# Performance work log

Hardware: AMD Instinct MI355X
Metric: run time of the kernel (lower is better)

Reference implementation:

```python
import jax, jax.numpy as jnp
import numpy as np

WS = 7           # window side
N = WS * WS      # tokens per window = 49
DIM = 384
H = 12
HD = DIM // H    # 32
BW = 2048        # num_windows * batch
NW = 4           # windows per image (mask batch)
SCALE = 1.0 / float(np.sqrt(HD))


def _rel_index():
    coords = np.stack(np.meshgrid(np.arange(WS), np.arange(WS), indexing='ij'))  # (2,7,7)
    flat = coords.reshape(2, -1)                      # (2,49)
    rel = flat[:, :, None] - flat[:, None, :]         # (2,49,49)
    rel = rel.transpose(1, 2, 0).copy()               # (49,49,2)
    rel[..., 0] += WS - 1
    rel[..., 1] += WS - 1
    rel[..., 0] *= 2 * WS - 1
    return jnp.asarray(rel.sum(-1), dtype=jnp.int32)  # (49,49)


def setup_inputs() -> dict:
    key = jax.random.key(0)
    ks = jax.random.split(key, 16)
    f32 = jnp.float32
    se = jax.random.normal(ks[0], (BW, N, DIM), dtype=f32)
    de = jax.random.normal(ks[1], (BW, N, DIM), dtype=f32)
    mask = jnp.where(jax.random.uniform(ks[2], (NW, N, N)) < 0.1, f32(-1e9), f32(0.0))
    s = 0.02
    w_v_se = jax.random.normal(ks[3], (DIM, DIM), dtype=f32) * s
    b_v_se = jnp.zeros((DIM,), dtype=f32)
    w_qkv = jax.random.normal(ks[4], (3 * DIM, DIM), dtype=f32) * s
    b_qkv = jnp.zeros((3 * DIM,), dtype=f32)
    w_proj_se = jax.random.normal(ks[5], (DIM, DIM), dtype=f32) * s
    b_proj_se = jnp.zeros((DIM,), dtype=f32)
    w_proj_de = jax.random.normal(ks[6], (DIM, DIM), dtype=f32) * s
    b_proj_de = jnp.zeros((DIM,), dtype=f32)
    rpb = jax.random.normal(ks[7], ((2 * WS - 1) ** 2, H), dtype=f32) * s  # (169,12)
    rel_idx = _rel_index()
    return {
        'se': se, 'de': de, 'mask': mask,
        'w_v_se': w_v_se, 'b_v_se': b_v_se,
        'w_qkv': w_qkv, 'b_qkv': b_qkv,
        'w_proj_se': w_proj_se, 'b_proj_se': b_proj_se,
        'w_proj_de': w_proj_de, 'b_proj_de': b_proj_de,
        'rpb': rpb, 'rel_idx': rel_idx,
    }


def reference(se, de, mask, w_v_se, b_v_se, w_qkv, b_qkv,
              w_proj_se, b_proj_se, w_proj_de, b_proj_de, rpb, rel_idx):
    B_, N_, C = se.shape
    # qkv from de (coa=False branch)
    qkv = (de @ w_qkv.T + b_qkv).reshape(B_, N_, 3, H, HD).transpose(2, 0, 3, 1, 4)
    q, k, v_de = qkv[0], qkv[1], qkv[2]                 # (B_,H,N,HD)
    v_se = (se @ w_v_se.T + b_v_se).reshape(B_, N_, H, HD).transpose(0, 2, 1, 3)
    attn = jnp.einsum('bhnd,bhmd->bhnm', q * SCALE, k)  # (B_,H,N,N)
    bias = rpb[rel_idx].transpose(2, 0, 1)              # (H,N,N)
    attn = attn + bias[None]
    # add window mask: view as (B, nW, H, N, N)
    attn = attn.reshape(B_ // NW, NW, H, N_, N_) + mask[None, :, None]
    attn = jax.nn.softmax(attn.reshape(B_, H, N_, N_), axis=-1)
    se_o = jnp.einsum('bhnm,bhmd->bnhd', attn, v_se).reshape(B_, N_, C)
    de_o = jnp.einsum('bhnm,bhmd->bnhd', attn, v_de).reshape(B_, N_, C)
    se_o = se_o @ w_proj_se.T + b_proj_se
    de_o = de_o @ w_proj_de.T + b_proj_de
    return (se_o, de_o)
```

## Files before the change

### kernel.cpp

```cpp
#include <hip/hip_runtime.h>

typedef _Float16 f16;
typedef __attribute__((ext_vector_type(8))) _Float16 f16x8;
typedef __attribute__((ext_vector_type(4))) _Float16 f16x4;
typedef __attribute__((ext_vector_type(4))) float f32x4;

#define MFMA16(a, b, c) __builtin_amdgcn_mfma_f32_16x16x32_f16(a, b, c, 0, 0, 0)

#define SCALE_F 0.17677669529663687f
#define NHEAD 12
#define NTOK 49
#define NBW 2048
#define VTJ 56

#define SB() __builtin_amdgcn_s_barrier()
#define SCHEDB() __builtin_amdgcn_sched_barrier(0)
#define WAITL0() asm volatile("s_waitcnt lgkmcnt(0)" ::: "memory")

__global__ void cast_weights(const float* __restrict__ wqkv, const float* __restrict__ wvse,
                             const float* __restrict__ wpse, const float* __restrict__ wpde,
                             f16* o_qkv, f16* o_vse, f16* o_pse, f16* o_pde) {
    int i = blockIdx.x * 256 + threadIdx.x;
    if (i >= 221184) return;
    const float* src;
    f16* dst;
    int off;
    if (i < 110592) { src = wqkv; dst = o_qkv; off = i; }
    else if (i < 147456) { src = wvse; dst = o_vse; off = i - 110592; }
    else if (i < 184320) { src = wpse; dst = o_pse; off = i - 147456; }
    else { src = wpde; dst = o_pde; off = i - 184320; }
    f32x4 v = ((const f32x4*)src)[off];
    f16x4 o;
#pragma unroll
    for (int e = 0; e < 4; ++e) o[e] = (f16)v[e];
    ((f16x4*)dst)[off] = o;
}

__global__ void prep_bm(const float* __restrict__ rpb, const int* __restrict__ rel_idx,
                        const float* __restrict__ mask, float* __restrict__ bm) {
    int blk = blockIdx.x;
    int w4 = blk / NHEAD, h = blk - w4 * NHEAD;
    for (int idx = threadIdx.x; idx < 4096; idx += 64) {
        int r = idx >> 6, c = idx & 63;
        float v = -1e30f;
        if (r < NTOK && c < NTOK)
            v = rpb[rel_idx[r * NTOK + c] * NHEAD + h] + mask[(w4 * NTOK + r) * NTOK + c];
        bm[(size_t)blk * 4096 + idx] = v;
    }
}

template <int EPI, bool A_F32, typename OUT_T>
__global__ __launch_bounds__(256) void gemm_bt(const void* __restrict__ Av, const f16* __restrict__ B,
                                               const float* __restrict__ bias, OUT_T* __restrict__ C,
                                               f16* __restrict__ VT, int N, int ldc) {
    __shared__ __align__(16) f16 As[128 * 64];
    __shared__ __align__(16) f16 Bs[128 * 64];
    const int nwg = gridDim.x * gridDim.y;
    int wg = blockIdx.y * gridDim.x + blockIdx.x;
    wg = (wg & 7) * (nwg >> 3) + (wg >> 3);
    const int m0 = (wg / gridDim.x) * 128, n0 = (wg % gridDim.x) * 128;
    const int tid = threadIdx.x;
    const int w = tid >> 6, l = tid & 63;
    const int wm = w >> 1, wn = w & 1;
    const int lr = l & 15, lg = l >> 4;
    const int sp = l & 7;
    const int lrow = l >> 3;

    f32x4 acc[4][4] = {};
    f32x4 t0[4], t1[4];
    f16x8 tf[4];

    auto LOADA = [&](int kt) {
#pragma unroll
        for (int it = 0; it < 4; ++it) {
            int row = w * 32 + it * 8 + lrow;
            if constexpr (A_F32) {
                const float* g = (const float*)Av + (size_t)(m0 + row) * 384 + kt * 64 + sp * 8;
                t0[it] = *(const f32x4*)g;
                t1[it] = *(const f32x4*)(g + 4);
            } else {
                tf[it] = *(const f16x8*)((const f16*)Av + (size_t)(m0 + row) * 384 + kt * 64 + sp * 8);
            }
        }
    };
    auto CVTWRITE = [&]() {
#pragma unroll
        for (int it = 0; it < 4; ++it) {
            int row = w * 32 + it * 8 + lrow;
            f16x8 hx;
            if constexpr (A_F32) {
#pragma unroll
                for (int e = 0; e < 4; ++e) { hx[e] = (f16)t0[it][e]; hx[e + 4] = (f16)t1[it][e]; }
            } else {
                hx = tf[it];
            }
            *(f16x8*)(As + row * 64 + (sp ^ (row & 7)) * 8) = hx;
        }
    };
    auto STAGEB = [&](int kt) {
#pragma unroll
        for (int it = 0; it < 4; ++it) {
            int row = w * 32 + it * 8 + lrow;
            int gchunk = sp ^ (row & 7);
            const f16* gB = B + (size_t)(n0 + row) * 384 + kt * 64 + gchunk * 8;
            f16* lB = Bs + (w * 32 + it * 8) * 64;
            __builtin_amdgcn_global_load_lds((const __attribute__((address_space(1))) void*)gB,
                                             (__attribute__((address_space(3))) void*)lB, 16, 0, 0);
        }
    };

    LOADA(0);
#pragma unroll
    for (int t = 0; t < 6; ++t) {
        WAITL0();
        SB();
        SCHEDB();
        CVTWRITE();
        STAGEB(t);
        if (t < 5) LOADA(t + 1);
        WAITL0();
        if (t < 5) {
            if constexpr (A_F32) asm volatile("s_waitcnt vmcnt(8)" ::: "memory");
            else asm volatile("s_waitcnt vmcnt(4)" ::: "memory");
        } else {
            asm volatile("s_waitcnt vmcnt(0)" ::: "memory");
        }
        SB();
        SCHEDB();
#pragma unroll
        for (int ks = 0; ks < 2; ++ks) {
            f16x8 af[4], bfr[4];
#pragma unroll
            for (int mi = 0; mi < 4; ++mi) {
                int r = 64 * wm + 16 * mi + lr;
                int chunk = (lg + 4 * ks) ^ (r & 7);
                af[mi] = *(const f16x8*)(As + r * 64 + chunk * 8);
            }
#pragma unroll
            for (int ni = 0; ni < 4; ++ni) {
                int r = 64 * wn + 16 * ni + lr;
                int chunk = (lg + 4 * ks) ^ (r & 7);
                bfr[ni] = *(const f16x8*)(Bs + r * 64 + chunk * 8);
            }
            __builtin_amdgcn_s_setprio(1);
#pragma unroll
            for (int mi = 0; mi < 4; ++mi)
#pragma unroll
                for (int ni = 0; ni < 4; ++ni)
                    acc[mi][ni] = MFMA16(af[mi], bfr[ni], acc[mi][ni]);
            __builtin_amdgcn_s_setprio(0);
        }
    }

#pragma unroll
    for (int mi = 0; mi < 4; ++mi) {
#pragma unroll
        for (int ni = 0; ni < 4; ++ni) {
            int col = n0 + 64 * wn + 16 * ni + lr;
            float bv = bias[col];
#pragma unroll
            for (int reg = 0; reg < 4; ++reg) {
                int row = m0 + 64 * wm + 16 * mi + 4 * lg + reg;
                float v = acc[mi][ni][reg] + bv;
                if constexpr (EPI == 0) {
                    C[(size_t)row * ldc + col] = (OUT_T)v;
                } else if constexpr (EPI == 1) {
                    if (col < 768) {
                        if (col < 384) v *= SCALE_F;
                        C[(size_t)row * 768 + col] = (OUT_T)v;
                    } else {
                        int c2 = col - 768;
                        int b = row / 49, j = row - b * 49;
                        VT[((size_t)b * NHEAD + (c2 >> 5)) * (32 * VTJ) + (c2 & 31) * VTJ + j] = (f16)v;
                    }
                } else {
                    int b = row / 49, j = row - b * 49;
                    VT[((size_t)b * NHEAD + (col >> 5)) * (32 * VTJ) + (col & 31) * VTJ + j] = (f16)v;
                }
            }
        }
    }
}

__global__ __launch_bounds__(128) void attn_kernel(const f16* __restrict__ qk,
                                                   const f16* __restrict__ vse_t,
                                                   const f16* __restrict__ vde_t,
                                                   const float* __restrict__ bm_all,
                                                   f16* __restrict__ att_se, f16* __restrict__ att_de) {
    __shared__ __align__(16) f16 Ps[2][64 * 64];

    const int wv = threadIdx.x >> 6;
    const int l = threadIdx.x & 63;
    const int bh = blockIdx.x * 2 + wv;
    const int b = bh / NHEAD, h = bh - b * NHEAD;
    const int lr = l & 15, lg = l >> 4;
    const size_t wbase = (size_t)b * NTOK;
    f16* P = Ps[wv];

    f16x8 qa[4], kb[4];
#pragma unroll
    for (int mi = 0; mi < 4; ++mi)
        qa[mi] = *(const f16x8*)(qk + (wbase + 16 * mi + lr) * 768 + h * 32 + lg * 8);
#pragma unroll
    for (int ni = 0; ni < 4; ++ni)
        kb[ni] = *(const f16x8*)(qk + (wbase + 16 * ni + lr) * 768 + 384 + h * 32 + lg * 8);

    const f32x4 zero4 = {0.f, 0.f, 0.f, 0.f};
    f32x4 S[4][4];
    __builtin_amdgcn_s_setprio(1);
#pragma unroll
    for (int mi = 0; mi < 4; ++mi)
#pragma unroll
        for (int ni = 0; ni < 4; ++ni)
            S[mi][ni] = MFMA16(qa[mi], kb[ni], zero4);
    __builtin_amdgcn_s_setprio(0);

    f16x8 vbr[2][2][2];
#pragma unroll
    for (int s = 0; s < 2; ++s) {
        const f16* vt = (s ? vde_t : vse_t) + (size_t)bh * (32 * VTJ);
#pragma unroll
        for (int ks = 0; ks < 2; ++ks)
#pragma unroll
            for (int ni = 0; ni < 2; ++ni) {
                int j0 = 8 * lg + 32 * ks;
                if (j0 == 56) j0 = 48;
                vbr[s][ks][ni] = *(const f16x8*)(vt + (16 * ni + lr) * VTJ + j0);
            }
    }

    const float* bmp = bm_all + (size_t)((b & 3) * NHEAD + h) * 4096;
#pragma unroll
    for (int mi = 0; mi < 4; ++mi) {
#pragma unroll
        for (int reg = 0; reg < 4; ++reg) {
            int r = 16 * mi + 4 * lg + reg;
            float v[4];
#pragma unroll
            for (int ni = 0; ni < 4; ++ni)
                v[ni] = S[mi][ni][reg] + bmp[(r << 6) + 16 * ni + lr];
            float mx = fmaxf(fmaxf(v[0], v[1]), fmaxf(v[2], v[3]));
#pragma unroll
            for (int off = 1; off < 16; off <<= 1) mx = fmaxf(mx, __shfl_xor(mx, off));
            float e[4];
            float sm = 0.f;
#pragma unroll
            for (int ni = 0; ni < 4; ++ni) {
                e[ni] = __expf(v[ni] - mx);
                sm += e[ni];
            }
#pragma unroll
            for (int off = 1; off < 16; off <<= 1) sm += __shfl_xor(sm, off);
            float inv = 1.f / sm;
#pragma unroll
            for (int ni = 0; ni < 4; ++ni)
                P[(r << 6) + ((16 * ni + lr) ^ ((r & 7) << 3))] = (f16)(e[ni] * inv);
        }
    }
    WAITL0();
    SCHEDB();

#pragma unroll
    for (int s = 0; s < 2; ++s) {
        f32x4 o[4][2] = {};
#pragma unroll
        for (int ks = 0; ks < 2; ++ks) {
            f16x8 pa[4];
#pragma unroll
            for (int mi = 0; mi < 4; ++mi) {
                int r = 16 * mi + lr;
                pa[mi] = *(const f16x8*)(P + (r << 6) + ((8 * lg + 32 * ks) ^ ((r & 7) << 3)));
            }
            __builtin_amdgcn_s_setprio(1);
#pragma unroll
            for (int ni = 0; ni < 2; ++ni)
#pragma unroll
                for (int mi = 0; mi < 4; ++mi) o[mi][ni] = MFMA16(pa[mi], vbr[s][ks][ni], o[mi][ni]);
            __builtin_amdgcn_s_setprio(0);
        }
        f16* dst = s ? att_de : att_se;
#pragma unroll
        for (int mi = 0; mi < 4; ++mi) {
#pragma unroll
            for (int reg = 0; reg < 4; ++reg) {
                int r = 16 * mi + 4 * lg + reg;
                if (r < NTOK) {
#pragma unroll
                    for (int ni = 0; ni < 2; ++ni)
                        dst[(wbase + r) * 384 + h * 32 + 16 * ni + lr] = (f16)o[mi][ni][reg];
                }
            }
        }
    }
}

extern "C" void kernel_launch(void* const* d_in, const int* in_sizes, int n_in,
                              void* d_out, int out_size, void* d_ws, size_t ws_size,
                              hipStream_t stream) {
    const float* se = (const float*)d_in[0];
    const float* de = (const float*)d_in[1];
    const float* mask = (const float*)d_in[2];
    const float* w_v_se = (const float*)d_in[3];
    const float* b_v_se = (const float*)d_in[4];
    const float* w_qkv = (const float*)d_in[5];
    const float* b_qkv = (const float*)d_in[6];
    const float* w_proj_se = (const float*)d_in[7];
    const float* b_proj_se = (const float*)d_in[8];
    const float* w_proj_de = (const float*)d_in[9];
    const float* b_proj_de = (const float*)d_in[10];
    const float* rpb = (const float*)d_in[11];
    const int* rel_idx = (const int*)d_in[12];

    const size_t SE_ELEMS = (size_t)NBW * NTOK * 384;

    char* ws = (char*)d_ws;
    f16* att_se = (f16*)(ws);
    f16* att_de = (f16*)(ws + 77070336);
    f16* qk_h   = (f16*)(ws + 154140672);
    f16* vse_t  = (f16*)(ws + 308281344);
    f16* vde_t  = (f16*)(ws + 396361728);
    f16* wqkv_h = (f16*)(ws + 484442112);
    f16* wvse_h = (f16*)(ws + 485326848);
    f16* wpse_h = (f16*)(ws + 485621760);
    f16* wpde_h = (f16*)(ws + 485916672);
    float* bm   = (float*)(ws + 486211584);

    cast_weights<<<864, 256, 0, stream>>>(w_qkv, w_v_se, w_proj_se, w_proj_de,
                                          wqkv_h, wvse_h, wpse_h, wpde_h);
    prep_bm<<<48, 64, 0, stream>>>(rpb, rel_idx, mask, bm);

    gemm_bt<1, true, f16><<<dim3(9, 784), 256, 0, stream>>>((const void*)de, wqkv_h, b_qkv,
                                                            qk_h, vde_t, 1152, 768);
    gemm_bt<2, true, f16><<<dim3(3, 784), 256, 0, stream>>>((const void*)se, wvse_h, b_v_se,
                                                            (f16*)nullptr, vse_t, 384, 384);

    attn_kernel<<<NBW * NHEAD / 2, 128, 0, stream>>>(qk_h, vse_t, vde_t, bm, att_se, att_de);

    gemm_bt<0, false, float><<<dim3(3, 784), 256, 0, stream>>>((const void*)att_se, wpse_h, b_proj_se,
                                                               (float*)d_out, nullptr, 384, 384);
    gemm_bt<0, false, float><<<dim3(3, 784), 256, 0, stream>>>((const void*)att_de, wpde_h, b_proj_de,
                                                               (float*)d_out + SE_ELEMS, nullptr, 384, 384);
}
```

Before: 697.6 us.

## Remove register prefetch pipeline in GEMM; use direct global-to-LDS loads for f16 A

The gemm_bt main loop drops its software pipelining, which prefetched the next A tile into registers while computing the current one. Each K-step now loads and converts A synchronously between two __syncthreads. For f16 A inputs, the A tile is also staged straight into LDS with global_load_lds, mirroring B, instead of going through registers. This cuts register pressure and the hand-written waitcnt logic, but global load latency is no longer overlapped with MFMA work.

```diff
diff --git a/kernel.cpp b/kernel.cpp
--- a/kernel.cpp
+++ b/kernel.cpp
@@ -13,7 +13,6 @@
 #define NBW 2048
 #define VTJ 56
 
-#define SB() __builtin_amdgcn_s_barrier()
 #define SCHEDB() __builtin_amdgcn_sched_barrier(0)
 #define WAITL0() asm volatile("s_waitcnt lgkmcnt(0)" ::: "memory")
 
@@ -67,66 +66,53 @@
     const int lrow = l >> 3;
 
     f32x4 acc[4][4] = {};
-    f32x4 t0[4], t1[4];
-    f16x8 tf[4];
-
-    auto LOADA = [&](int kt) {
-#pragma unroll
-        for (int it = 0; it < 4; ++it) {
-            int row = w * 32 + it * 8 + lrow;
-            if constexpr (A_F32) {
-                const float* g = (const float*)Av + (size_t)(m0 + row) * 384 + kt * 64 + sp * 8;
+
+    for (int t = 0; t < 6; ++t) {
+        __syncthreads();
+        if constexpr (A_F32) {
+            const float* A32 = (const float*)Av;
+            f32x4 t0[4], t1[4];
+#pragma unroll
+            for (int it = 0; it < 4; ++it) {
+                int row = w * 32 + it * 8 + lrow;
+                const float* g = A32 + (size_t)(m0 + row) * 384 + t * 64 + sp * 8;
                 t0[it] = *(const f32x4*)g;
                 t1[it] = *(const f32x4*)(g + 4);
-            } else {
-                tf[it] = *(const f16x8*)((const f16*)Av + (size_t)(m0 + row) * 384 + kt * 64 + sp * 8);
-            }
-        }
-    };
-    auto CVTWRITE = [&]() {
-#pragma unroll
-        for (int it = 0; it < 4; ++it) {
-            int row = w * 32 + it * 8 + lrow;
-            f16x8 hx;
-            if constexpr (A_F32) {
+            }
+#pragma unroll
+            for (int it = 0; it < 4; ++it) {
+                int row = w * 32 + it * 8 + lrow;
+                f16x8 hx;
 #pragma unroll
                 for (int e = 0; e < 4; ++e) { hx[e] = (f16)t0[it][e]; hx[e + 4] = (f16)t1[it][e]; }
-            } else {
-                hx = tf[it];
-            }
-            *(f16x8*)(As + row * 64 + (sp ^ (row & 7)) * 8) = hx;
-        }
-    };
-    auto STAGEB = [&](int kt) {
-#pragma unroll
-        for (int it = 0; it < 4; ++it) {
-            int row = w * 32 + it * 8 + lrow;
-            int gchunk = sp ^ (row & 7);
-            const f16* gB = B + (size_t)(n0 + row) * 384 + kt * 64 + gchunk * 8;
-            f16* lB = Bs + (w * 32 + it * 8) * 64;
-            __builtin_amdgcn_global_load_lds((const __attribute__((address_space(1))) void*)gB,
-                                             (__attribute__((address_space(3))) void*)lB, 16, 0, 0);
-        }
-    };
-
-    LOADA(0);
-#pragma unroll
-    for (int t = 0; t < 6; ++t) {
-        WAITL0();
-        SB();
-        SCHEDB();
-        CVTWRITE();
-        STAGEB(t);
-        if (t < 5) LOADA(t + 1);
-        WAITL0();
-        if (t < 5) {
-            if constexpr (A_F32) asm volatile("s_waitcnt vmcnt(8)" ::: "memory");
-            else asm volatile("s_waitcnt vmcnt(4)" ::: "memory");
+                *(f16x8*)(As + row * 64 + (sp ^ (row & 7)) * 8) = hx;
+            }
+#pragma unroll
+            for (int it = 0; it < 4; ++it) {
+                int row = w * 32 + it * 8 + lrow;
+                int gchunk = sp ^ (row & 7);
+                const f16* gB = B + (size_t)(n0 + row) * 384 + t * 64 + gchunk * 8;
+                f16* lB = Bs + (w * 32 + it * 8) * 64;
+                __builtin_amdgcn_global_load_lds((const __attribute__((address_space(1))) void*)gB,
+                                                 (__attribute__((address_space(3))) void*)lB, 16, 0, 0);
+            }
         } else {
-            asm volatile("s_waitcnt vmcnt(0)" ::: "memory");
-        }
-        SB();
-        SCHEDB();
+            const f16* A16 = (const f16*)Av;
+#pragma unroll
+            for (int it = 0; it < 4; ++it) {
+                int row = w * 32 + it * 8 + lrow;
+                int gchunk = sp ^ (row & 7);
+                const f16* gA = A16 + (size_t)(m0 + row) * 384 + t * 64 + gchunk * 8;
+                const f16* gB = B + (size_t)(n0 + row) * 384 + t * 64 + gchunk * 8;
+                f16* lA = As + (w * 32 + it * 8) * 64;
+                f16* lB = Bs + (w * 32 + it * 8) * 64;
+                __builtin_amdgcn_global_load_lds((const __attribute__((address_space(1))) void*)gA,
+                                                 (__attribute__((address_space(3))) void*)lA, 16, 0, 0);
+                __builtin_amdgcn_global_load_lds((const __attribute__((address_space(1))) void*)gB,
+                                                 (__attribute__((address_space(3))) void*)lB, 16, 0, 0);
+            }
+        }
+        __syncthreads();
 #pragma unroll
         for (int ks = 0; ks < 2; ++ks) {
             f16x8 af[4], bfr[4];
```

Result: slower. 714.9 us (+2.5%).
